# Optimization experiments

Measured on AMD Instinct MI355X. Metric: run time of the kernel, lower is better.

## Reference

```python
import jax, jax.numpy as jnp
import numpy as np

B, S, D, O, C = 4, 2048, 1024, 1024, 8


def setup_inputs() -> dict:
    key = jax.random.key(0)
    k1, k2, k3, k4 = jax.random.split(key, 4)
    x = jax.random.normal(k1, (B, S, D), dtype=jnp.float32)
    category_id = jax.random.randint(k2, (B, S), 0, C, dtype=jnp.int64)
    weight = jax.random.normal(k3, (C, D, O), dtype=jnp.float32)
    bias = jax.random.normal(k4, (C, O), dtype=jnp.float32)
    return {"x": x, "category_id": category_id, "weight": weight, "bias": bias}


def reference(x, category_id, weight, bias):
    # Faithful to: out[t] = x[t] @ weight[cid[t]] + bias[cid[t]]
    # Instead of gathering a full [T, D, O] weight tensor per token (32GB),
    # compute every category's projection once and select per token.
    orig_shape = x.shape
    x_flat = x.reshape(-1, orig_shape[-1])          # [T, D]
    cid = category_id.reshape(-1)                    # [T]
    out_all = jnp.einsum('td,cdo->tco', x_flat, weight)  # [T, C, O]
    out = jnp.take_along_axis(out_all, cid[:, None, None], axis=1)[:, 0, :]  # [T, O]
    out = out + bias[cid]
    return out.reshape(orig_shape[:-1] + (weight.shape[-1],))
```

## Files before the change

### kernel.cpp

```cpp
#include <hip/hip_runtime.h>

#define TOK   8192
#define DIM   1024
#define OUTD  1024
#define NCAT  8
#define BM    128
#define BN    128
#define BK    32
#define MAX_MT 71
#define MPMAX (MAX_MT * BM)

typedef __attribute__((ext_vector_type(8))) __bf16 bf16x8;
typedef __attribute__((ext_vector_type(4))) float  f32x4;

__device__ __forceinline__ unsigned short f2bf(float f) {
  unsigned u = __float_as_uint(f);
  u += 0x7fffu + ((u >> 16) & 1u);
  return (unsigned short)(u >> 16);
}

__global__ __launch_bounds__(1024) void k_build(const int* __restrict__ cid,
    int* __restrict__ row_token, int* __restrict__ tile_c, int* __restrict__ tile_m) {
  __shared__ int cnt[NCAT], gbase[NCAT], pos[NCAT];
  int tid = threadIdx.x;
  if (tid < NCAT) { cnt[tid] = 0; pos[tid] = 0; }
  __syncthreads();
  for (int t = tid; t < TOK; t += 1024) atomicAdd(&cnt[cid[t]], 1);
  __syncthreads();
  if (tid == 0) {
    int mt = 0, pr = 0;
    for (int c = 0; c < NCAT; ++c) {
      gbase[c] = pr;
      int nt = (cnt[c] + BM - 1) / BM;
      for (int i = 0; i < nt; ++i) { tile_c[mt] = c; tile_m[mt] = pr + i * BM; ++mt; }
      pr += nt * BM;
    }
    for (; mt < MAX_MT; ++mt) { tile_c[mt] = -1; tile_m[mt] = 0; }
  }
  __syncthreads();
  for (int r = tid; r < MPMAX; r += 1024) row_token[r] = -1;
  __syncthreads();
  for (int t = tid; t < TOK; t += 1024) {
    int c = cid[t];
    int p = atomicAdd(&pos[c], 1);
    row_token[gbase[c] + p] = t;
  }
}

__global__ __launch_bounds__(256) void k_gather_x(const float* __restrict__ x,
    const int* __restrict__ row_token, unsigned short* __restrict__ xg) {
  int idx = blockIdx.x * 256 + threadIdx.x;
  int r  = idx >> 7;
  int e0 = (idx & 127) << 3;
  if (r >= MPMAX) return;
  int tok = row_token[r];
  union { unsigned short u[8]; uint4 v; } o;
  if (tok >= 0) {
    const float4* s = (const float4*)(x + (size_t)tok * DIM + e0);
    float4 a = s[0], b = s[1];
    o.u[0] = f2bf(a.x); o.u[1] = f2bf(a.y); o.u[2] = f2bf(a.z); o.u[3] = f2bf(a.w);
    o.u[4] = f2bf(b.x); o.u[5] = f2bf(b.y); o.u[6] = f2bf(b.z); o.u[7] = f2bf(b.w);
  } else {
    o.v = make_uint4(0u, 0u, 0u, 0u);
  }
  *(uint4*)(xg + (size_t)r * DIM + e0) = o.v;
}

__global__ __launch_bounds__(256) void k_conv_w(const float* __restrict__ w,
    unsigned short* __restrict__ wt) {
  int c = blockIdx.z, dt = blockIdx.y, ot = blockIdx.x;
  __shared__ unsigned short t[64][72];
  int tid = threadIdx.x;
  int i  = tid >> 2;
  int jg = tid & 3;
  const float* src = w + ((size_t)c << 20) + (size_t)(dt * 64 + i) * 1024 + ot * 64 + jg * 16;
  #pragma unroll
  for (int q = 0; q < 4; ++q) {
    float4 v = *(const float4*)(src + q * 4);
    t[jg * 16 + q * 4 + 0][i] = f2bf(v.x);
    t[jg * 16 + q * 4 + 1][i] = f2bf(v.y);
    t[jg * 16 + q * 4 + 2][i] = f2bf(v.z);
    t[jg * 16 + q * 4 + 3][i] = f2bf(v.w);
  }
  __syncthreads();
  unsigned short* dst = wt + ((size_t)c << 20) + (size_t)(ot * 64 + i) * 1024 + dt * 64 + jg * 16;
  uint4 a = *(const uint4*)&t[i][jg * 16];
  uint4 b = *(const uint4*)&t[i][jg * 16 + 8];
  *(uint4*)dst = a;
  *(uint4*)(dst + 8) = b;
}

__global__ __launch_bounds__(256) void k_gemm(const unsigned short* __restrict__ xg,
    const unsigned short* __restrict__ wt, const float* __restrict__ bias,
    const int* __restrict__ row_token, const int* __restrict__ tile_c,
    const int* __restrict__ tile_m, float* __restrict__ out) {
  int mt = blockIdx.y;
  int c = tile_c[mt];
  if (c < 0) return;
  int m0 = tile_m[mt];
  int n0 = blockIdx.x * BN;

  __shared__ unsigned short As[BM][BK];
  __shared__ unsigned short Bs[BN][BK];

  int tid  = threadIdx.x;
  int lane = tid & 63;
  int wave = tid >> 6;
  int wr = wave >> 1, wc = wave & 1;

  f32x4 acc[4][4];
  #pragma unroll
  for (int m = 0; m < 4; ++m)
    #pragma unroll
    for (int n = 0; n < 4; ++n) acc[m][n] = (f32x4){0.f, 0.f, 0.f, 0.f};

  const unsigned short* Ag = xg + (size_t)m0 * DIM;
  const unsigned short* Bg = wt + ((size_t)c << 20) + (size_t)n0 * DIM;
  int srow = tid >> 2;
  int scol = (tid & 3) << 3;

  for (int kt = 0; kt < DIM; kt += BK) {
    __syncthreads();
    __builtin_amdgcn_global_load_lds(
      (const __attribute__((address_space(1))) unsigned int*)(Ag + (size_t)srow * DIM + kt + scol),
      (__attribute__((address_space(3))) unsigned int*)(&As[srow][scol]), 16, 0, 0);
    __builtin_amdgcn_global_load_lds(
      (const __attribute__((address_space(1))) unsigned int*)(Ag + (size_t)(srow + 64) * DIM + kt + scol),
      (__attribute__((address_space(3))) unsigned int*)(&As[srow + 64][scol]), 16, 0, 0);
    __builtin_amdgcn_global_load_lds(
      (const __attribute__((address_space(1))) unsigned int*)(Bg + (size_t)srow * DIM + kt + scol),
      (__attribute__((address_space(3))) unsigned int*)(&Bs[srow][scol]), 16, 0, 0);
    __builtin_amdgcn_global_load_lds(
      (const __attribute__((address_space(1))) unsigned int*)(Bg + (size_t)(srow + 64) * DIM + kt + scol),
      (__attribute__((address_space(3))) unsigned int*)(&Bs[srow + 64][scol]), 16, 0, 0);
    __syncthreads();

    bf16x8 a[4], b[4];
    #pragma unroll
    for (int m = 0; m < 4; ++m)
      a[m] = *(const bf16x8*)&As[wr * 64 + m * 16 + (lane & 15)][(lane >> 4) * 8];
    #pragma unroll
    for (int n = 0; n < 4; ++n)
      b[n] = *(const bf16x8*)&Bs[wc * 64 + n * 16 + (lane & 15)][(lane >> 4) * 8];
    #pragma unroll
    for (int m = 0; m < 4; ++m)
      #pragma unroll
      for (int n = 0; n < 4; ++n)
        acc[m][n] = __builtin_amdgcn_mfma_f32_16x16x32_bf16(a[m], b[n], acc[m][n], 0, 0, 0);
  }

  int col = lane & 15;
  int rq  = (lane >> 4) << 2;
  float bv[4];
  #pragma unroll
  for (int n = 0; n < 4; ++n) bv[n] = bias[c * OUTD + n0 + wc * 64 + n * 16 + col];
  #pragma unroll
  for (int m = 0; m < 4; ++m) {
    #pragma unroll
    for (int r = 0; r < 4; ++r) {
      int prow = m0 + wr * 64 + m * 16 + rq + r;
      int tok = row_token[prow];
      if (tok < 0) continue;
      float* orow = out + (size_t)tok * OUTD + n0 + wc * 64 + col;
      #pragma unroll
      for (int n = 0; n < 4; ++n) orow[n * 16] = acc[m][n][r] + bv[n];
    }
  }
}

extern "C" void kernel_launch(void* const* d_in, const int* in_sizes, int n_in,
                              void* d_out, int out_size, void* d_ws, size_t ws_size,
                              hipStream_t stream) {
  const float* x    = (const float*)d_in[0];
  const int*   cid  = (const int*)d_in[1];
  const float* w    = (const float*)d_in[2];
  const float* bias = (const float*)d_in[3];
  float* out = (float*)d_out;

  char* ws = (char*)d_ws;
  constexpr size_t XG_BYTES = (size_t)MPMAX * DIM * 2;
  constexpr size_t WT_BYTES = (size_t)NCAT * DIM * OUTD * 2;
  constexpr size_t RT_BYTES = (size_t)MPMAX * 4;
  unsigned short* xg  = (unsigned short*)ws;
  unsigned short* wtb = (unsigned short*)(ws + XG_BYTES);
  int* row_token = (int*)(ws + XG_BYTES + WT_BYTES);
  int* tile_c    = (int*)(ws + XG_BYTES + WT_BYTES + RT_BYTES);
  int* tile_m    = tile_c + MAX_MT;

  k_build<<<1, 1024, 0, stream>>>(cid, row_token, tile_c, tile_m);
  k_conv_w<<<dim3(16, 16, NCAT), 256, 0, stream>>>(w, wtb);
  k_gather_x<<<(MPMAX * (DIM / 8) + 255) / 256, 256, 0, stream>>>(x, row_token, xg);
  k_gemm<<<dim3(OUTD / BN, MAX_MT), 256, 0, stream>>>(xg, wtb, bias, row_token, tile_c, tile_m, out);
}
```

Before: 155.5 us.

## Double-buffer GEMM LDS tiles, fuse conversion kernels, use ballot-based bucketing

```diff
diff --git a/kernel.cpp b/kernel.cpp
--- a/kernel.cpp
+++ b/kernel.cpp
@@ -21,17 +21,39 @@
 
 __global__ __launch_bounds__(1024) void k_build(const int* __restrict__ cid,
     int* __restrict__ row_token, int* __restrict__ tile_c, int* __restrict__ tile_m) {
-  __shared__ int cnt[NCAT], gbase[NCAT], pos[NCAT];
-  int tid = threadIdx.x;
-  if (tid < NCAT) { cnt[tid] = 0; pos[tid] = 0; }
-  __syncthreads();
-  for (int t = tid; t < TOK; t += 1024) atomicAdd(&cnt[cid[t]], 1);
-  __syncthreads();
+  __shared__ int wcnt[16][NCAT];
+  __shared__ int wbase[16][NCAT];
+  __shared__ int gbase[NCAT];
+  int tid = threadIdx.x, lane = tid & 63, wave = tid >> 6;
+  int base = wave * 512;
+
+  int cs[8];
+  #pragma unroll
+  for (int it = 0; it < 8; ++it) cs[it] = cid[base + it * 64 + lane];
+  int cnt_loc[NCAT];
+  #pragma unroll
+  for (int c = 0; c < NCAT; ++c) cnt_loc[c] = 0;
+  #pragma unroll
+  for (int it = 0; it < 8; ++it) {
+    #pragma unroll
+    for (int c = 0; c < NCAT; ++c) {
+      unsigned long long m = __ballot(cs[it] == c);
+      cnt_loc[c] += __popcll(m);
+    }
+  }
+  if (lane == 0) {
+    #pragma unroll
+    for (int c = 0; c < NCAT; ++c) wcnt[wave][c] = cnt_loc[c];
+  }
+  __syncthreads();
+
   if (tid == 0) {
-    int mt = 0, pr = 0;
+    int pr = 0, mt = 0;
     for (int c = 0; c < NCAT; ++c) {
+      int tot = 0;
+      for (int w = 0; w < 16; ++w) { wbase[w][c] = tot; tot += wcnt[w][c]; }
       gbase[c] = pr;
-      int nt = (cnt[c] + BM - 1) / BM;
+      int nt = (tot + BM - 1) / BM;
       for (int i = 0; i < nt; ++i) { tile_c[mt] = c; tile_m[mt] = pr + i * BM; ++mt; }
       pr += nt * BM;
     }
@@ -40,54 +62,68 @@
   __syncthreads();
   for (int r = tid; r < MPMAX; r += 1024) row_token[r] = -1;
   __syncthreads();
-  for (int t = tid; t < TOK; t += 1024) {
-    int c = cid[t];
-    int p = atomicAdd(&pos[c], 1);
-    row_token[gbase[c] + p] = t;
-  }
-}
-
-__global__ __launch_bounds__(256) void k_gather_x(const float* __restrict__ x,
-    const int* __restrict__ row_token, unsigned short* __restrict__ xg) {
-  int idx = blockIdx.x * 256 + threadIdx.x;
-  int r  = idx >> 7;
-  int e0 = (idx & 127) << 3;
-  if (r >= MPMAX) return;
-  int tok = row_token[r];
-  union { unsigned short u[8]; uint4 v; } o;
-  if (tok >= 0) {
-    const float4* s = (const float4*)(x + (size_t)tok * DIM + e0);
-    float4 a = s[0], b = s[1];
-    o.u[0] = f2bf(a.x); o.u[1] = f2bf(a.y); o.u[2] = f2bf(a.z); o.u[3] = f2bf(a.w);
-    o.u[4] = f2bf(b.x); o.u[5] = f2bf(b.y); o.u[6] = f2bf(b.z); o.u[7] = f2bf(b.w);
+
+  int run[NCAT];
+  #pragma unroll
+  for (int c = 0; c < NCAT; ++c) run[c] = gbase[c] + wbase[wave][c];
+  unsigned long long lt = (lane == 63) ? ~0ull >> 1 : ((1ull << lane) - 1);
+  #pragma unroll
+  for (int it = 0; it < 8; ++it) {
+    int t = base + it * 64 + lane;
+    int c = cs[it];
+    int pos = 0;
+    #pragma unroll
+    for (int cat = 0; cat < NCAT; ++cat) {
+      unsigned long long m = __ballot(cs[it] == cat);
+      if (cat == c) pos = run[cat] + __popcll(m & lt);
+      run[cat] += __popcll(m);
+    }
+    row_token[pos] = t;
+  }
+}
+
+__global__ __launch_bounds__(256) void k_convert(const float* __restrict__ w,
+    const float* __restrict__ x, const int* __restrict__ row_token,
+    unsigned short* __restrict__ wt, unsigned short* __restrict__ xg) {
+  int tid = threadIdx.x;
+  if (blockIdx.x < 2048) {
+    int b = blockIdx.x;
+    int ot = b & 15, dt = (b >> 4) & 15, c = b >> 8;
+    __shared__ unsigned short t[64][72];
+    int i  = tid >> 2;
+    int jg = tid & 3;
+    const float* src = w + ((size_t)c << 20) + (size_t)(dt * 64 + i) * 1024 + ot * 64 + jg * 16;
+    #pragma unroll
+    for (int q = 0; q < 4; ++q) {
+      float4 v = *(const float4*)(src + q * 4);
+      t[jg * 16 + q * 4 + 0][i] = f2bf(v.x);
+      t[jg * 16 + q * 4 + 1][i] = f2bf(v.y);
+      t[jg * 16 + q * 4 + 2][i] = f2bf(v.z);
+      t[jg * 16 + q * 4 + 3][i] = f2bf(v.w);
+    }
+    __syncthreads();
+    unsigned short* dst = wt + ((size_t)c << 20) + (size_t)(ot * 64 + i) * 1024 + dt * 64 + jg * 16;
+    uint4 a = *(const uint4*)&t[i][jg * 16];
+    uint4 bq = *(const uint4*)&t[i][jg * 16 + 8];
+    *(uint4*)dst = a;
+    *(uint4*)(dst + 8) = bq;
   } else {
-    o.v = make_uint4(0u, 0u, 0u, 0u);
-  }
-  *(uint4*)(xg + (size_t)r * DIM + e0) = o.v;
-}
-
-__global__ __launch_bounds__(256) void k_conv_w(const float* __restrict__ w,
-    unsigned short* __restrict__ wt) {
-  int c = blockIdx.z, dt = blockIdx.y, ot = blockIdx.x;
-  __shared__ unsigned short t[64][72];
-  int tid = threadIdx.x;
-  int i  = tid >> 2;
-  int jg = tid & 3;
-  const float* src = w + ((size_t)c << 20) + (size_t)(dt * 64 + i) * 1024 + ot * 64 + jg * 16;
-  #pragma unroll
-  for (int q = 0; q < 4; ++q) {
-    float4 v = *(const float4*)(src + q * 4);
-    t[jg * 16 + q * 4 + 0][i] = f2bf(v.x);
-    t[jg * 16 + q * 4 + 1][i] = f2bf(v.y);
-    t[jg * 16 + q * 4 + 2][i] = f2bf(v.z);
-    t[jg * 16 + q * 4 + 3][i] = f2bf(v.w);
-  }
-  __syncthreads();
-  unsigned short* dst = wt + ((size_t)c << 20) + (size_t)(ot * 64 + i) * 1024 + dt * 64 + jg * 16;
-  uint4 a = *(const uint4*)&t[i][jg * 16];
-  uint4 b = *(const uint4*)&t[i][jg * 16 + 8];
-  *(uint4*)dst = a;
-  *(uint4*)(dst + 8) = b;
+    int idx = (blockIdx.x - 2048) * 256 + tid;
+    int r  = idx >> 7;
+    int e0 = (idx & 127) << 3;
+    if (r >= MPMAX) return;
+    int tok = row_token[r];
+    union { unsigned short u[8]; uint4 v; } o;
+    if (tok >= 0) {
+      const float4* s = (const float4*)(x + (size_t)tok * DIM + e0);
+      float4 a = s[0], b = s[1];
+      o.u[0] = f2bf(a.x); o.u[1] = f2bf(a.y); o.u[2] = f2bf(a.z); o.u[3] = f2bf(a.w);
+      o.u[4] = f2bf(b.x); o.u[5] = f2bf(b.y); o.u[6] = f2bf(b.z); o.u[7] = f2bf(b.w);
+    } else {
+      o.v = make_uint4(0u, 0u, 0u, 0u);
+    }
+    *(uint4*)(xg + (size_t)r * DIM + e0) = o.v;
+  }
 }
 
 __global__ __launch_bounds__(256) void k_gemm(const unsigned short* __restrict__ xg,
@@ -100,8 +136,8 @@
   int m0 = tile_m[mt];
   int n0 = blockIdx.x * BN;
 
-  __shared__ unsigned short As[BM][BK];
-  __shared__ unsigned short Bs[BN][BK];
+  __shared__ unsigned short As[2][BM][BK];
+  __shared__ unsigned short Bs[2][BM][BK];
 
   int tid  = threadIdx.x;
   int lane = tid & 63;
@@ -119,29 +155,50 @@
   int srow = tid >> 2;
   int scol = (tid & 3) << 3;
 
-  for (int kt = 0; kt < DIM; kt += BK) {
+  auto STAGE = [&](int buf, int kt) {
+    __builtin_amdgcn_global_load_lds(
+      (const __attribute__((address_space(1))) unsigned int*)(Ag + (size_t)srow * DIM + kt + scol),
+      (__attribute__((address_space(3))) unsigned int*)(&As[buf][srow][scol]), 16, 0, 0);
+    __builtin_amdgcn_global_load_lds(
+      (const __attribute__((address_space(1))) unsigned int*)(Ag + (size_t)(srow + 64) * DIM + kt + scol),
+      (__attribute__((address_space(3))) unsigned int*)(&As[buf][srow + 64][scol]), 16, 0, 0);
+    __builtin_amdgcn_global_load_lds(
+      (const __attribute__((address_space(1))) unsigned int*)(Bg + (size_t)srow * DIM + kt + scol),
+      (__attribute__((address_space(3))) unsigned int*)(&Bs[buf][srow][scol]), 16, 0, 0);
+    __builtin_amdgcn_global_load_lds(
+      (const __attribute__((address_space(1))) unsigned int*)(Bg + (size_t)(srow + 64) * DIM + kt + scol),
+      (__attribute__((address_space(3))) unsigned int*)(&Bs[buf][srow + 64][scol]), 16, 0, 0);
+  };
+
+  STAGE(0, 0);
+  __syncthreads();
+
+  int cur = 0;
+  for (int kt = 0; kt < DIM - BK; kt += BK) {
+    STAGE(cur ^ 1, kt + BK);
+    bf16x8 a[4], b[4];
+    #pragma unroll
+    for (int m = 0; m < 4; ++m)
+      a[m] = *(const bf16x8*)&As[cur][wr * 64 + m * 16 + (lane & 15)][(lane >> 4) * 8];
+    #pragma unroll
+    for (int n = 0; n < 4; ++n)
+      b[n] = *(const bf16x8*)&Bs[cur][wc * 64 + n * 16 + (lane & 15)][(lane >> 4) * 8];
+    #pragma unroll
+    for (int m = 0; m < 4; ++m)
+      #pragma unroll
+      for (int n = 0; n < 4; ++n)
+        acc[m][n] = __builtin_amdgcn_mfma_f32_16x16x32_bf16(a[m], b[n], acc[m][n], 0, 0, 0);
     __syncthreads();
-    __builtin_amdgcn_global_load_lds(
-      (const __attribute__((address_space(1))) unsigned int*)(Ag + (size_t)srow * DIM + kt + scol),
-      (__attribute__((address_space(3))) unsigned int*)(&As[srow][scol]), 16, 0, 0);
-    __builtin_amdgcn_global_load_lds(
-      (const __attribute__((address_space(1))) unsigned int*)(Ag + (size_t)(srow + 64) * DIM + kt + scol),
-      (__attribute__((address_space(3))) unsigned int*)(&As[srow + 64][scol]), 16, 0, 0);
-    __builtin_amdgcn_global_load_lds(
-      (const __attribute__((address_space(1))) unsigned int*)(Bg + (size_t)srow * DIM + kt + scol),
-      (__attribute__((address_space(3))) unsigned int*)(&Bs[srow][scol]), 16, 0, 0);
-    __builtin_amdgcn_global_load_lds(
-      (const __attribute__((address_space(1))) unsigned int*)(Bg + (size_t)(srow + 64) * DIM + kt + scol),
-      (__attribute__((address_space(3))) unsigned int*)(&Bs[srow + 64][scol]), 16, 0, 0);
-    __syncthreads();
-
+    cur ^= 1;
+  }
+  {
     bf16x8 a[4], b[4];
     #pragma unroll
     for (int m = 0; m < 4; ++m)
-      a[m] = *(const bf16x8*)&As[wr * 64 + m * 16 + (lane & 15)][(lane >> 4) * 8];
+      a[m] = *(const bf16x8*)&As[cur][wr * 64 + m * 16 + (lane & 15)][(lane >> 4) * 8];
     #pragma unroll
     for (int n = 0; n < 4; ++n)
-      b[n] = *(const bf16x8*)&Bs[wc * 64 + n * 16 + (lane & 15)][(lane >> 4) * 8];
+      b[n] = *(const bf16x8*)&Bs[cur][wc * 64 + n * 16 + (lane & 15)][(lane >> 4) * 8];
     #pragma unroll
     for (int m = 0; m < 4; ++m)
       #pragma unroll
@@ -188,7 +245,6 @@
   int* tile_m    = tile_c + MAX_MT;
 
   k_build<<<1, 1024, 0, stream>>>(cid, row_token, tile_c, tile_m);
-  k_conv_w<<<dim3(16, 16, NCAT), 256, 0, stream>>>(w, wtb);
-  k_gather_x<<<(MPMAX * (DIM / 8) + 255) / 256, 256, 0, stream>>>(x, row_token, xg);
+  k_convert<<<2048 + (MPMAX * (DIM / 8) + 255) / 256, 256, 0, stream>>>(w, x, row_token, wtb, xg);
   k_gemm<<<dim3(OUTD / BN, MAX_MT), 256, 0, stream>>>(xg, wtb, bias, row_token, tile_c, tile_m, out);
 }
```

Result: slower. 161.3 us (+3.7%).
